# Performance work log

Hardware: AMD Instinct MI355X
Metric: run time of the kernel (lower is better)

Reference implementation:

```python
import jax, jax.numpy as jnp
import numpy as np

VOCAB = 32000
DIM = 64


def setup_inputs() -> dict:
    key = jax.random.key(0)
    k1, k2 = jax.random.split(key)
    sequence = jax.random.randint(k1, (16, 2048), 0, VOCAB, dtype=jnp.int64 if jax.config.jax_enable_x64 else jnp.int32)
    weight = jax.random.normal(k2, (VOCAB, DIM), dtype=jnp.float32)
    return {"sequence": sequence, "weight": weight}


def reference(sequence, weight):
    # Embedding gather: [B, S, D]
    embs = weight[sequence]
    # Pairwise synergy bias: [B, S, S], scaled dot product
    bias = jnp.einsum('bsd,btd->bst', embs, embs) / jnp.sqrt(jnp.asarray(DIM, embs.dtype))
    return bias
```

## Files before the change

### kernel.cpp

```cpp
#include <hip/hip_runtime.h>
#include <hip/hip_bf16.h>

#define VOCAB 32000
#define DIM 64
#define NB 16
#define SEQ 2048

typedef __attribute__((ext_vector_type(8))) short bf16x8;
typedef __attribute__((ext_vector_type(4))) float f32x4;

__device__ __forceinline__ unsigned short f2bf(float f) {
    unsigned int u = __builtin_bit_cast(unsigned int, f);
    u = (u + 0x7fffu + ((u >> 16) & 1u)) >> 16;
    return (unsigned short)u;
}

__global__ __launch_bounds__(256) void gather_cvt(
        const int* __restrict__ seq,
        const float* __restrict__ weight,
        unsigned short* __restrict__ embs) {
    int tid = blockIdx.x * 256 + threadIdx.x;
    int token = tid >> 3;
    int c = (tid & 7) * 8;
    int row = seq[token];
    const float* src = weight + (size_t)row * DIM + c;
    unsigned short o[8];
#pragma unroll
    for (int j = 0; j < 8; ++j) o[j] = f2bf(src[j]);
    *reinterpret_cast<bf16x8*>(embs + (size_t)token * DIM + c) =
        *reinterpret_cast<bf16x8*>(o);
}

__global__ __launch_bounds__(256) void synergy_gemm(
        const unsigned short* __restrict__ embs,
        float* __restrict__ out) {
    const int b    = blockIdx.z;
    const int n0   = blockIdx.x * 128;
    const int wave = threadIdx.x >> 6;
    const int lane = threadIdx.x & 63;
    const int m0   = blockIdx.y * 128 + wave * 32;
    const int r    = lane & 15;
    const int q    = lane >> 4;

    const unsigned short* eb = embs + (size_t)b * SEQ * DIM;

    bf16x8 a[2][2], bv[8][2];
#pragma unroll
    for (int mt = 0; mt < 2; ++mt) {
        const unsigned short* p = eb + (size_t)(m0 + mt * 16 + r) * DIM + q * 8;
        a[mt][0] = *reinterpret_cast<const bf16x8*>(p);
        a[mt][1] = *reinterpret_cast<const bf16x8*>(p + 32);
    }
#pragma unroll
    for (int nt = 0; nt < 8; ++nt) {
        const unsigned short* p = eb + (size_t)(n0 + nt * 16 + r) * DIM + q * 8;
        bv[nt][0] = *reinterpret_cast<const bf16x8*>(p);
        bv[nt][1] = *reinterpret_cast<const bf16x8*>(p + 32);
    }

    f32x4 acc[2][8];
#pragma unroll
    for (int mt = 0; mt < 2; ++mt)
#pragma unroll
        for (int nt = 0; nt < 8; ++nt) {
            f32x4 c = {0.f, 0.f, 0.f, 0.f};
            c = __builtin_amdgcn_mfma_f32_16x16x32_bf16(a[mt][0], bv[nt][0], c, 0, 0, 0);
            c = __builtin_amdgcn_mfma_f32_16x16x32_bf16(a[mt][1], bv[nt][1], c, 0, 0, 0);
            acc[mt][nt] = c;
        }

    float* ob = out + (size_t)b * SEQ * SEQ;
#pragma unroll
    for (int nt = 0; nt < 8; ++nt) {
        size_t rowoff = (size_t)(n0 + nt * 16 + r) * SEQ;
#pragma unroll
        for (int mt = 0; mt < 2; ++mt) {
            f32x4 v = acc[mt][nt] * 0.125f;
            *reinterpret_cast<f32x4*>(ob + rowoff + (m0 + mt * 16 + q * 4)) = v;
        }
    }
}

extern "C" void kernel_launch(void* const* d_in, const int* in_sizes, int n_in,
                              void* d_out, int out_size, void* d_ws, size_t ws_size,
                              hipStream_t stream) {
    const int*   seq    = (const int*)d_in[0];
    const float* weight = (const float*)d_in[1];
    float*       out    = (float*)d_out;
    unsigned short* embs = (unsigned short*)d_ws;

    gather_cvt<<<dim3(262144 / 256), dim3(256), 0, stream>>>(seq, weight, embs);

    synergy_gemm<<<dim3(SEQ / 128, SEQ / 128, NB), dim3(256), 0, stream>>>(embs, out);
}
```

Before: 292.6 us.

## Restructure synergy GEMM into row strips with per-wave column sweeps

Each block now owns a 16-row strip of one batch, and each wave sweeps 512 output columns in 16-column steps. Operands are loaded per step and results are written as scalar stores, where the old version used 128x128 tiles with vectorized f32x4 stores. The intent is a more sequential, row-contiguous write pattern for the large fp32 output and higher occupancy via launch bounds. The cost is scalar stores, less register reuse of B operands, and more repeated global loads of embeddings.

```diff
diff --git a/kernel.cpp b/kernel.cpp
--- a/kernel.cpp
+++ b/kernel.cpp
@@ -31,53 +31,41 @@
         *reinterpret_cast<bf16x8*>(o);
 }
 
-__global__ __launch_bounds__(256) void synergy_gemm(
+__global__ __launch_bounds__(256, 8) void synergy_gemm(
         const unsigned short* __restrict__ embs,
         float* __restrict__ out) {
-    const int b    = blockIdx.z;
-    const int n0   = blockIdx.x * 128;
-    const int wave = threadIdx.x >> 6;
-    const int lane = threadIdx.x & 63;
-    const int m0   = blockIdx.y * 128 + wave * 32;
-    const int r    = lane & 15;
-    const int q    = lane >> 4;
+    const int b     = blockIdx.y;
+    const int strip = blockIdx.x;
+    const int wave  = threadIdx.x >> 6;
+    const int lane  = threadIdx.x & 63;
+    const int r     = lane & 15;
+    const int q     = lane >> 4;
+    const int m0    = strip * 16;
+    const int nc0   = wave * 512;
 
     const unsigned short* eb = embs + (size_t)b * SEQ * DIM;
 
-    bf16x8 a[2][2], bv[8][2];
+    const unsigned short* pa = eb + (size_t)(m0 + r) * DIM + q * 8;
+    const bf16x8 a0 = *reinterpret_cast<const bf16x8*>(pa);
+    const bf16x8 a1 = *reinterpret_cast<const bf16x8*>(pa + 32);
+
+    const unsigned short* pb = eb + (size_t)(nc0 + r) * DIM + q * 8;
+
+    float* o = out + (size_t)b * SEQ * SEQ + (size_t)(m0 + q * 4) * SEQ
+                   + nc0 + r;
+
+#pragma unroll 4
+    for (int it = 0; it < 32; ++it) {
+        bf16x8 b0 = *reinterpret_cast<const bf16x8*>(pb);
+        bf16x8 b1 = *reinterpret_cast<const bf16x8*>(pb + 32);
+        f32x4 c = {0.f, 0.f, 0.f, 0.f};
+        c = __builtin_amdgcn_mfma_f32_16x16x32_bf16(a0, b0, c, 0, 0, 0);
+        c = __builtin_amdgcn_mfma_f32_16x16x32_bf16(a1, b1, c, 0, 0, 0);
+        float* oc = o + it * 16;
 #pragma unroll
-    for (int mt = 0; mt < 2; ++mt) {
-        const unsigned short* p = eb + (size_t)(m0 + mt * 16 + r) * DIM + q * 8;
-        a[mt][0] = *reinterpret_cast<const bf16x8*>(p);
-        a[mt][1] = *reinterpret_cast<const bf16x8*>(p + 32);
-    }
-#pragma unroll
-    for (int nt = 0; nt < 8; ++nt) {
-        const unsigned short* p = eb + (size_t)(n0 + nt * 16 + r) * DIM + q * 8;
-        bv[nt][0] = *reinterpret_cast<const bf16x8*>(p);
-        bv[nt][1] = *reinterpret_cast<const bf16x8*>(p + 32);
-    }
-
-    f32x4 acc[2][8];
-#pragma unroll
-    for (int mt = 0; mt < 2; ++mt)
-#pragma unroll
-        for (int nt = 0; nt < 8; ++nt) {
-            f32x4 c = {0.f, 0.f, 0.f, 0.f};
-            c = __builtin_amdgcn_mfma_f32_16x16x32_bf16(a[mt][0], bv[nt][0], c, 0, 0, 0);
-            c = __builtin_amdgcn_mfma_f32_16x16x32_bf16(a[mt][1], bv[nt][1], c, 0, 0, 0);
-            acc[mt][nt] = c;
-        }
-
-    float* ob = out + (size_t)b * SEQ * SEQ;
-#pragma unroll
-    for (int nt = 0; nt < 8; ++nt) {
-        size_t rowoff = (size_t)(n0 + nt * 16 + r) * SEQ;
-#pragma unroll
-        for (int mt = 0; mt < 2; ++mt) {
-            f32x4 v = acc[mt][nt] * 0.125f;
-            *reinterpret_cast<f32x4*>(ob + rowoff + (m0 + mt * 16 + q * 4)) = v;
-        }
+        for (int reg = 0; reg < 4; ++reg)
+            oc[(size_t)reg * SEQ] = c[reg] * 0.125f;
+        pb += 16 * DIM;
     }
 }
 
@@ -91,5 +79,5 @@
 
     gather_cvt<<<dim3(262144 / 256), dim3(256), 0, stream>>>(seq, weight, embs);
 
-    synergy_gemm<<<dim3(SEQ / 128, SEQ / 128, NB), dim3(256), 0, stream>>>(embs, out);
+    synergy_gemm<<<dim3(SEQ / 16, NB), dim3(256), 0, stream>>>(embs, out);
 }
```

After: 303.8 us. 3.8% more time.
